# Kernel optimization log

Measured on AMD Instinct MI355X. Metric: run time of the kernel, lower is better.

Reference implementation:

```python
import jax, jax.numpy as jnp
import numpy as np

N_NODES = 100000


def _gcn_layer(x, W, b, src, dst, ew):
    # support = x @ W  (dense transform first, standard GCN)
    support = x @ W  # [N, out]
    # sparse propagate: out[i] = sum_{e: dst[e]=i} ew[e] * support[src[e]]
    msgs = support[src] * ew[:, None]  # [E, out]
    out = jax.ops.segment_sum(msgs, dst, num_segments=N_NODES)
    return out + b


def setup_inputs() -> dict:
    key = jax.random.key(0)
    ks = jax.random.split(key, 7)
    nfeat, nhid, nclass, E = 512, 256, 40, 3200000
    x = jax.random.normal(ks[0], (N_NODES, nfeat), dtype=jnp.float32)
    edge_index = jax.random.randint(ks[1], (2, E), 0, N_NODES, dtype=jnp.int32)
    edge_weight = jax.random.uniform(ks[2], (E,), dtype=jnp.float32)
    W1 = jax.random.normal(ks[3], (nfeat, nhid), dtype=jnp.float32) / np.sqrt(nfeat)
    b1 = jnp.zeros((nhid,), dtype=jnp.float32)
    W2 = jax.random.normal(ks[4], (nhid, nclass), dtype=jnp.float32) / np.sqrt(nhid)
    b2 = jnp.zeros((nclass,), dtype=jnp.float32)
    return {"x": x, "edge_index": edge_index, "edge_weight": edge_weight,
            "W1": W1, "b1": b1, "W2": W2, "b2": b2}


def reference(x, edge_index, edge_weight, W1, b1, W2, b2):
    src, dst = edge_index[0], edge_index[1]
    h = _gcn_layer(x, W1, b1, src, dst, edge_weight)
    h = jax.nn.relu(h)  # with_relu=True; dropout skipped (eval mode)
    h = _gcn_layer(h, W2, b2, src, dst, edge_weight)
    return jax.nn.log_softmax(h, axis=1)
```

## Files before the change

kernel.cpp:

```cpp
#include <hip/hip_runtime.h>
#include <math.h>

#define N_NODES 100000
#define M_PAD 100096
#define NFEAT 512
#define NHID 256
#define NCLASS 40
#define SUP2_LD 48

#define NBKT 250
#define NPB 400
#define BINA_CHUNK 3072
#define BCAP 14336

typedef __attribute__((ext_vector_type(8))) short bf16x8;
typedef __attribute__((ext_vector_type(4))) float f32x4;

__device__ __forceinline__ unsigned short f2bf(float f) {
    unsigned int u = __builtin_bit_cast(unsigned int, f);
    u += 0x7fffu + ((u >> 16) & 1u);
    return (unsigned short)(u >> 16);
}
__device__ __forceinline__ void bf2x2(unsigned int u, float& f0, float& f1) {
    f0 = __builtin_bit_cast(float, u << 16);
    f1 = __builtin_bit_cast(float, u & 0xffff0000u);
}
__device__ __forceinline__ void gload16(const void* g, void* l) {
    __builtin_amdgcn_global_load_lds(
        (const __attribute__((address_space(1))) unsigned int*)g,
        (__attribute__((address_space(3))) unsigned int*)l, 16, 0, 0);
}
template <int CODE>
__device__ __forceinline__ float swzx(float v) {
    return __builtin_bit_cast(float,
        __builtin_amdgcn_ds_swizzle(__builtin_bit_cast(int, v), CODE));
}

#define CVTW_BLOCKS 512

__global__ __launch_bounds__(256) void k_init(int* __restrict__ bcur,
                                              const float* __restrict__ W1,
                                              unsigned short* __restrict__ w1t,
                                              const float* __restrict__ W2,
                                              uint4* __restrict__ w2f) {
    int b = blockIdx.x;
    int t = threadIdx.x;
    if (b == 0) {
        if (t < NBKT) bcur[t] = t * BCAP;
    } else if (b <= CVTW_BLOCKS) {
        int idx = (b - 1) * 256 + t;
        int n = idx >> 9, k = idx & 511;
        w1t[idx] = f2bf(W1[(size_t)k * NHID + n]);
    } else {
        for (int idx = t; idx < 8 * 3 * 64; idx += 256) {
            int ks = idx / 192;
            int rem = idx - ks * 192;
            int n = rem >> 6;
            int l = rem & 63;
            int col = n * 16 + (l & 15);
            int kbase = ks * 32 + (l >> 4) * 8;
            unsigned short o[8];
#pragma unroll
            for (int j = 0; j < 8; ++j)
                o[j] = (col < NCLASS) ? f2bf(W2[(size_t)(kbase + j) * NCLASS + col]) : 0;
            w2f[idx] = *(const uint4*)o;
        }
    }
}

__device__ __forceinline__ void binA_body(char* smbase, int t, int cblk,
                                          const int* __restrict__ src,
                                          const int* __restrict__ dst,
                                          const float* __restrict__ ew,
                                          int* __restrict__ bcur,
                                          uint2* __restrict__ tmp, int E) {
    uint2* sorted = (uint2*)smbase;
    unsigned char* bkt8 = (unsigned char*)(smbase + 24576);
    int* cnt = (int*)(smbase + 27648);
    int* startv = cnt + 256;
    int* offv = startv + 256;
    int* gb = offv + 256;
    int c0 = cblk * BINA_CHUNK;
    int n = min(BINA_CHUNK, E - c0);
    cnt[t] = 0;
    __syncthreads();
    for (int j = t; j < n; j += 256) {
        atomicAdd(&cnt[(unsigned)dst[c0 + j] / NPB], 1);
    }
    __syncthreads();
    int v = cnt[t];
    startv[t] = v;
    __syncthreads();
    for (int o = 1; o < 256; o <<= 1) {
        int a = (t >= o) ? startv[t - o] : 0;
        __syncthreads();
        startv[t] += a;
        __syncthreads();
    }
    int ex = startv[t] - v;
    __syncthreads();
    startv[t] = ex;
    offv[t] = ex;
    if (t < NBKT) gb[t] = (v > 0) ? atomicAdd(&bcur[t], v) : 0;
    __syncthreads();
    for (int j = t; j < n; j += 256) {
        int d = dst[c0 + j];
        int b = (unsigned)d / NPB;
        int dl = d - b * NPB;
        int r = atomicAdd(&offv[b], 1);
        sorted[r] = make_uint2((unsigned)src[c0 + j] | ((unsigned)dl << 17),
                               __builtin_bit_cast(unsigned, ew[c0 + j]));
        bkt8[r] = (unsigned char)b;
    }
    __syncthreads();
    for (int j = t; j < n; j += 256) {
        int b = bkt8[j];
        tmp[gb[b] + (j - startv[b])] = sorted[j];
    }
}

__device__ __forceinline__ void gemm1_body(char* smem, int t, int mb,
                                           const float* __restrict__ x,
                                           const unsigned short* __restrict__ w1t,
                                           unsigned short* __restrict__ sup1) {
    const int w = t >> 6, lane = t & 63;
    const int m0 = mb * 128;
    const int wm = w >> 1, wn = w & 1;
    const int r15 = lane & 15, hi = lane >> 4;

    f32x4 acc[4][8];
#pragma unroll
    for (int i = 0; i < 4; ++i)
#pragma unroll
        for (int j = 0; j < 8; ++j) acc[i][j] = (f32x4){0.f, 0.f, 0.f, 0.f};

    const char* wsrc = (const char*)w1t;

#define STAGE1(kt, b)                                                                  \
    {                                                                                  \
        char* Ab = smem + (b) * 8192;                                                  \
        char* Bb = smem + 16384 + (b) * 16384;                                         \
        _Pragma("unroll") for (int i = 0; i < 2; ++i) {                                \
            int u = i * 256 + t;                                                       \
            int row = u >> 2, part = u & 3;                                            \
            int gr = m0 + row;                                                         \
            unsigned short ob[8];                                                      \
            if (gr < N_NODES) {                                                        \
                const float* sp = x + (size_t)gr * NFEAT + (kt) * 32 + part * 8;       \
                float4 v0 = *(const float4*)sp;                                        \
                float4 v1 = *(const float4*)(sp + 4);                                  \
                ob[0] = f2bf(v0.x); ob[1] = f2bf(v0.y);                                \
                ob[2] = f2bf(v0.z); ob[3] = f2bf(v0.w);                                \
                ob[4] = f2bf(v1.x); ob[5] = f2bf(v1.y);                                \
                ob[6] = f2bf(v1.z); ob[7] = f2bf(v1.w);                                \
            } else {                                                                   \
                _Pragma("unroll") for (int j = 0; j < 8; ++j) ob[j] = 0;               \
            }                                                                          \
            *(uint4*)(Ab + row * 64 + ((part ^ ((row >> 1) & 3)) << 4)) =              \
                *(const uint4*)ob;                                                     \
        }                                                                              \
        _Pragma("unroll") for (int i = 0; i < 4; ++i) {                                \
            int u = i * 256 + t;                                                       \
            int nrow = u >> 2, part = u & 3;                                           \
            int q = part ^ ((nrow >> 1) & 3);                                          \
            gload16(wsrc + (size_t)nrow * 1024 + (kt) * 64 + q * 16, Bb + u * 16);     \
        }                                                                              \
    }

    STAGE1(0, 0);
    for (int kt = 0; kt < 16; ++kt) {
        __syncthreads();
        if (kt < 15) STAGE1(kt + 1, (kt + 1) & 1);
        const char* Ab = smem + (kt & 1) * 8192;
        const char* Bb = smem + 16384 + (kt & 1) * 16384;
        bf16x8 a[4], bb[8];
#pragma unroll
        for (int i = 0; i < 4; ++i) {
            int r = wm * 64 + i * 16 + r15;
            a[i] = *(const bf16x8*)(Ab + r * 64 + ((hi ^ ((r >> 1) & 3)) << 4));
        }
#pragma unroll
        for (int j = 0; j < 8; ++j) {
            int n = wn * 128 + j * 16 + r15;
            bb[j] = *(const bf16x8*)(Bb + n * 64 + ((hi ^ ((n >> 1) & 3)) << 4));
        }
#pragma unroll
        for (int i = 0; i < 4; ++i)
#pragma unroll
            for (int j = 0; j < 8; ++j)
                acc[i][j] = __builtin_amdgcn_mfma_f32_16x16x32_bf16(a[i], bb[j], acc[i][j], 0, 0, 0);
    }
#undef STAGE1

#pragma unroll
    for (int i = 0; i < 4; ++i) {
        int rowb = m0 + wm * 64 + i * 16 + hi * 4;
#pragma unroll
        for (int j = 0; j < 8; ++j) {
            int col = wn * 128 + j * 16 + r15;
#pragma unroll
            for (int r = 0; r < 4; ++r)
                sup1[(size_t)(rowb + r) * NHID + col] = f2bf(acc[i][j][r]);
        }
    }
}

#define GEMM1_BLOCKS (M_PAD / 128)

__global__ __launch_bounds__(256) void k_fat(const float* __restrict__ x,
                                             const unsigned short* __restrict__ w1t,
                                             unsigned short* __restrict__ sup1,
                                             const int* __restrict__ src,
                                             const int* __restrict__ dst,
                                             const float* __restrict__ ew,
                                             int* __restrict__ bcur,
                                             uint2* __restrict__ tmp, int E) {
    __shared__ __align__(16) char smem[49152];
    int b = blockIdx.x;
    int t = threadIdx.x;
    if (b < GEMM1_BLOCKS) {
        gemm1_body(smem, t, b, x, w1t, sup1);
    } else {
        binA_body(smem, t, b - GEMM1_BLOCKS, src, dst, ew, bcur, tmp, E);
    }
}

__global__ __launch_bounds__(256) void k_binB(const uint2* __restrict__ tmp,
                                              const int* __restrict__ bcur,
                                              int* __restrict__ rowptr,
                                              uint2* __restrict__ cedge) {
    __shared__ int sc[256];
    __shared__ int nc[NPB];
    __shared__ int st[NPB];
    int b = blockIdx.x, t = threadIdx.x;
    int c = (t < NBKT) ? (bcur[t] - t * BCAP) : 0;
    sc[t] = c;
    __syncthreads();
    for (int o = 1; o < 256; o <<= 1) {
        int a = (t >= o) ? sc[t - o] : 0;
        __syncthreads();
        sc[t] += a;
        __syncthreads();
    }
    int base = (b == 0) ? 0 : sc[b - 1];
    int mycnt = sc[b] - base;
    int total = sc[NBKT - 1];
    __syncthreads();
    for (int i = t; i < NPB; i += 256) nc[i] = 0;
    __syncthreads();
    const uint2* srcp = tmp + (size_t)b * BCAP;
    for (int j = t; j < mycnt; j += 256) atomicAdd(&nc[srcp[j].x >> 17], 1);
    __syncthreads();
    int v0 = nc[t];
    sc[t] = v0;
    __syncthreads();
    for (int o = 1; o < 256; o <<= 1) {
        int a = (t >= o) ? sc[t - o] : 0;
        __syncthreads();
        sc[t] += a;
        __syncthreads();
    }
    int tot0 = sc[255];
    st[t] = sc[t] - v0;
    __syncthreads();
    int v1 = (t < NPB - 256) ? nc[256 + t] : 0;
    sc[t] = v1;
    __syncthreads();
    for (int o = 1; o < 256; o <<= 1) {
        int a = (t >= o) ? sc[t - o] : 0;
        __syncthreads();
        sc[t] += a;
        __syncthreads();
    }
    if (t < NPB - 256) st[256 + t] = tot0 + sc[t] - v1;
    __syncthreads();
    int n0 = b * NPB;
    for (int i = t; i < NPB; i += 256) {
        int s = base + st[i];
        rowptr[n0 + i] = s;
        st[i] = s;
    }
    if (b == NBKT - 1 && t == 0) rowptr[N_NODES] = total;
    __syncthreads();
    for (int j = t; j < mycnt; j += 256) {
        uint2 e = srcp[j];
        int dl = e.x >> 17;
        int addr = atomicAdd(&st[dl], 1);
        cedge[addr] = make_uint2(e.x & 0x1FFFFu, e.y);
    }
}

__global__ __launch_bounds__(256) void k_prop1(const unsigned short* __restrict__ sup1,
                                               const int* __restrict__ rowptr,
                                               const uint2* __restrict__ cedge,
                                               const float* __restrict__ b1,
                                               unsigned short* __restrict__ h1) {
    int gid = blockIdx.x * blockDim.x + threadIdx.x;
    int wid = gid >> 6;
    int lane = gid & 63;
    if (wid >= N_NODES) return;
    int beg = rowptr[wid], end = rowptr[wid + 1];
    float a0 = 0.f, a1 = 0.f, a2 = 0.f, a3 = 0.f;
    int e = beg;
    for (; e + 7 < end; e += 8) {
        uint2 ed[8];
#pragma unroll
        for (int q = 0; q < 8; ++q) ed[q] = cedge[e + q];
        uint2 r[8];
#pragma unroll
        for (int q = 0; q < 8; ++q)
            r[q] = *(const uint2*)(sup1 + (size_t)ed[q].x * NHID + lane * 4);
#pragma unroll
        for (int q = 0; q < 8; ++q) {
            float wq = __builtin_bit_cast(float, ed[q].y);
            float f0, f1, f2, f3;
            bf2x2(r[q].x, f0, f1);
            bf2x2(r[q].y, f2, f3);
            a0 += wq * f0; a1 += wq * f1; a2 += wq * f2; a3 += wq * f3;
        }
    }
    for (; e < end; ++e) {
        uint2 ed = cedge[e];
        float wq = __builtin_bit_cast(float, ed.y);
        uint2 rv = *(const uint2*)(sup1 + (size_t)ed.x * NHID + lane * 4);
        float f0, f1, f2, f3;
        bf2x2(rv.x, f0, f1);
        bf2x2(rv.y, f2, f3);
        a0 += wq * f0; a1 += wq * f1; a2 += wq * f2; a3 += wq * f3;
    }
    float4 bv = *(const float4*)(b1 + lane * 4);
    a0 = fmaxf(a0 + bv.x, 0.f);
    a1 = fmaxf(a1 + bv.y, 0.f);
    a2 = fmaxf(a2 + bv.z, 0.f);
    a3 = fmaxf(a3 + bv.w, 0.f);
    unsigned short o[4] = {f2bf(a0), f2bf(a1), f2bf(a2), f2bf(a3)};
    *(uint2*)(h1 + (size_t)wid * NHID + lane * 4) = *(const uint2*)o;
}

__global__ __launch_bounds__(256) void k_gemm2(const unsigned short* __restrict__ h1,
                                               const uint4* __restrict__ w2f,
                                               unsigned short* __restrict__ sup2) {
    int t = threadIdx.x;
    int w = t >> 6, lane = t & 63;
    int m0 = (blockIdx.x * 4 + w) * 16;
    int r15 = lane & 15, hi = lane >> 4;

    bf16x8 bfrag[8][3];
#pragma unroll
    for (int ks = 0; ks < 8; ++ks)
#pragma unroll
        for (int n = 0; n < 3; ++n)
            bfrag[ks][n] = __builtin_bit_cast(bf16x8, w2f[(ks * 3 + n) * 64 + lane]);

    f32x4 acc[3];
#pragma unroll
    for (int n = 0; n < 3; ++n) acc[n] = (f32x4){0.f, 0.f, 0.f, 0.f};

    const unsigned short* arow = h1 + (size_t)(m0 + r15) * NHID + hi * 8;
#pragma unroll
    for (int ks = 0; ks < 8; ++ks) {
        bf16x8 a = *(const bf16x8*)(arow + ks * 32);
#pragma unroll
        for (int n = 0; n < 3; ++n)
            acc[n] = __builtin_amdgcn_mfma_f32_16x16x32_bf16(a, bfrag[ks][n], acc[n], 0, 0, 0);
    }
#pragma unroll
    for (int n = 0; n < 3; ++n) {
        int col = n * 16 + r15;
#pragma unroll
        for (int r = 0; r < 4; ++r) {
            int row = m0 + hi * 4 + r;
            sup2[(size_t)row * SUP2_LD + col] = f2bf(acc[n][r]);
        }
    }
}

__global__ __launch_bounds__(256) void k_prop2(const unsigned short* __restrict__ sup2,
                                               const int* __restrict__ rowptr,
                                               const uint2* __restrict__ cedge,
                                               const float* __restrict__ b2,
                                               float* __restrict__ out) {
    int gid = blockIdx.x * blockDim.x + threadIdx.x;
    int wv = gid >> 6;
    int lane = gid & 63;
    int grp = lane >> 5;
    int l32 = lane & 31;
    int wid = wv * 2 + grp;
    if (wid >= N_NODES) return;
    int beg = rowptr[wid], end = rowptr[wid + 1];
    bool act = l32 < 20;
    int c2 = l32 * 2;
    float acc0 = 0.f, acc1 = 0.f;
    int e = beg;
    for (; e + 7 < end; e += 8) {
        uint2 ed[8];
#pragma unroll
        for (int q = 0; q < 8; ++q) ed[q] = cedge[e + q];
        unsigned u[8];
#pragma unroll
        for (int q = 0; q < 8; ++q)
            u[q] = act ? *(const unsigned*)(sup2 + (size_t)ed[q].x * SUP2_LD + c2) : 0u;
#pragma unroll
        for (int q = 0; q < 8; ++q) {
            float wq = __builtin_bit_cast(float, ed[q].y);
            float f0, f1;
            bf2x2(u[q], f0, f1);
            acc0 += wq * f0;
            acc1 += wq * f1;
        }
    }
    for (; e < end; ++e) {
        uint2 eq = cedge[e];
        unsigned u = act ? *(const unsigned*)(sup2 + (size_t)eq.x * SUP2_LD + c2) : 0u;
        float wq = __builtin_bit_cast(float, eq.y);
        float f0, f1;
        bf2x2(u, f0, f1);
        acc0 += wq * f0;
        acc1 += wq * f1;
    }
    float v0 = -INFINITY, v1 = -INFINITY;
    if (act) {
        float2 bb = *(const float2*)(b2 + c2);
        v0 = acc0 + bb.x;
        v1 = acc1 + bb.y;
    }
    float m = fmaxf(v0, v1);
    m = fmaxf(m, swzx<0x401F>(m));
    m = fmaxf(m, swzx<0x201F>(m));
    m = fmaxf(m, swzx<0x101F>(m));
    m = fmaxf(m, swzx<0x081F>(m));
    m = fmaxf(m, swzx<0x041F>(m));
    float s = act ? (expf(v0 - m) + expf(v1 - m)) : 0.f;
    s += swzx<0x401F>(s);
    s += swzx<0x201F>(s);
    s += swzx<0x101F>(s);
    s += swzx<0x081F>(s);
    s += swzx<0x041F>(s);
    if (act) {
        float ls = logf(s);
        float2 o = make_float2(v0 - m - ls, v1 - m - ls);
        *(float2*)(out + (size_t)wid * NCLASS + c2) = o;
    }
}


extern "C" void kernel_launch(void* const* d_in, const int* in_sizes, int n_in,
                              void* d_out, int out_size, void* d_ws, size_t ws_size,
                              hipStream_t stream) {
    const float* x = (const float*)d_in[0];
    const int* ei = (const int*)d_in[1];
    const float* ew = (const float*)d_in[2];
    const float* W1 = (const float*)d_in[3];
    const float* b1 = (const float*)d_in[4];
    const float* W2 = (const float*)d_in[5];
    const float* b2 = (const float*)d_in[6];
    float* out = (float*)d_out;

    int E = in_sizes[1] / 2;
    const int* src = ei;
    const int* dst = ei + E;

    char* w = (char*)d_ws;
    size_t off = 0;
    auto alloc = [&](size_t bytes) {
        void* p = w + off;
        off += (bytes + 255) & ~(size_t)255;
        return p;
    };
    unsigned short* w1t = (unsigned short*)alloc((size_t)NHID * NFEAT * 2);
    unsigned short* sup1 = (unsigned short*)alloc((size_t)M_PAD * NHID * 2);
    unsigned short* h1 = (unsigned short*)alloc((size_t)M_PAD * NHID * 2);
    uint2* cedge = (uint2*)alloc((size_t)E * 8);
    uint2* tmp = (uint2*)alloc((size_t)NBKT * BCAP * 8);
    unsigned short* sup2 = (unsigned short*)alloc((size_t)M_PAD * SUP2_LD * 2);
    int* rowptr = (int*)alloc((size_t)(N_NODES + 1) * 4);
    int* bcur = (int*)alloc((size_t)NBKT * 4);
    uint4* w2f = (uint4*)alloc((size_t)8 * 3 * 64 * 16);

    const int BINA_BLOCKS = (E + BINA_CHUNK - 1) / BINA_CHUNK;

    k_init<<<1 + CVTW_BLOCKS + 1, 256, 0, stream>>>(bcur, W1, w1t, W2, w2f);
    k_fat<<<GEMM1_BLOCKS + BINA_BLOCKS, 256, 0, stream>>>(x, w1t, sup1,
                                                          src, dst, ew, bcur, tmp, E);
    k_binB<<<NBKT, 256, 0, stream>>>(tmp, bcur, rowptr, cedge);
    k_prop1<<<(N_NODES + 3) / 4, 256, 0, stream>>>(sup1, rowptr, cedge, b1, h1);
    k_gemm2<<<M_PAD / 64, 256, 0, stream>>>(h1, w2f, sup2);
    k_prop2<<<(N_NODES / 2 + 3) / 4, 256, 0, stream>>>(sup2, rowptr, cedge, b2, out);
}
```

Baseline: 506.2 us.

## Give GEMM1 blocks two tiles each and pack four nodes per wave in prop2

```diff
diff --git a/kernel.cpp b/kernel.cpp
--- a/kernel.cpp
+++ b/kernel.cpp
@@ -12,6 +12,9 @@
 #define NPB 400
 #define BINA_CHUNK 3072
 #define BCAP 14336
+
+#define GEMM1_TILES 782
+#define GEMM1_BLOCKS 391
 
 typedef __attribute__((ext_vector_type(8))) short bf16x8;
 typedef __attribute__((ext_vector_type(4))) float f32x4;
@@ -205,8 +208,6 @@
     }
 }
 
-#define GEMM1_BLOCKS (M_PAD / 128)
-
 __global__ __launch_bounds__(256) void k_fat(const float* __restrict__ x,
                                              const unsigned short* __restrict__ w1t,
                                              unsigned short* __restrict__ sup1,
@@ -220,6 +221,8 @@
     int t = threadIdx.x;
     if (b < GEMM1_BLOCKS) {
         gemm1_body(smem, t, b, x, w1t, sup1);
+        __syncthreads();
+        gemm1_body(smem, t, b + GEMM1_BLOCKS, x, w1t, sup1);
     } else {
         binA_body(smem, t, b - GEMM1_BLOCKS, src, dst, ew, bcur, tmp, E);
     }
@@ -383,63 +386,65 @@
     int gid = blockIdx.x * blockDim.x + threadIdx.x;
     int wv = gid >> 6;
     int lane = gid & 63;
-    int grp = lane >> 5;
-    int l32 = lane & 31;
-    int wid = wv * 2 + grp;
+    int grp = lane >> 4;
+    int gl = lane & 15;
+    int wid = wv * 4 + grp;
     if (wid >= N_NODES) return;
     int beg = rowptr[wid], end = rowptr[wid + 1];
-    bool act = l32 < 20;
-    int c2 = l32 * 2;
-    float acc0 = 0.f, acc1 = 0.f;
+    bool act = gl < 10;
+    int c4 = gl * 4;
+    float acc0 = 0.f, acc1 = 0.f, acc2 = 0.f, acc3 = 0.f;
     int e = beg;
     for (; e + 7 < end; e += 8) {
         uint2 ed[8];
 #pragma unroll
         for (int q = 0; q < 8; ++q) ed[q] = cedge[e + q];
-        unsigned u[8];
+        uint2 u[8];
 #pragma unroll
         for (int q = 0; q < 8; ++q)
-            u[q] = act ? *(const unsigned*)(sup2 + (size_t)ed[q].x * SUP2_LD + c2) : 0u;
+            u[q] = act ? *(const uint2*)(sup2 + (size_t)ed[q].x * SUP2_LD + c4)
+                       : make_uint2(0u, 0u);
 #pragma unroll
         for (int q = 0; q < 8; ++q) {
             float wq = __builtin_bit_cast(float, ed[q].y);
-            float f0, f1;
-            bf2x2(u[q], f0, f1);
-            acc0 += wq * f0;
-            acc1 += wq * f1;
+            float f0, f1, f2, f3;
+            bf2x2(u[q].x, f0, f1);
+            bf2x2(u[q].y, f2, f3);
+            acc0 += wq * f0; acc1 += wq * f1; acc2 += wq * f2; acc3 += wq * f3;
         }
     }
     for (; e < end; ++e) {
         uint2 eq = cedge[e];
-        unsigned u = act ? *(const unsigned*)(sup2 + (size_t)eq.x * SUP2_LD + c2) : 0u;
+        uint2 u = act ? *(const uint2*)(sup2 + (size_t)eq.x * SUP2_LD + c4)
+                      : make_uint2(0u, 0u);
         float wq = __builtin_bit_cast(float, eq.y);
-        float f0, f1;
-        bf2x2(u, f0, f1);
-        acc0 += wq * f0;
-        acc1 += wq * f1;
-    }
-    float v0 = -INFINITY, v1 = -INFINITY;
+        float f0, f1, f2, f3;
+        bf2x2(u.x, f0, f1);
+        bf2x2(u.y, f2, f3);
+        acc0 += wq * f0; acc1 += wq * f1; acc2 += wq * f2; acc3 += wq * f3;
+    }
+    float v0 = -INFINITY, v1 = -INFINITY, v2 = -INFINITY, v3 = -INFINITY;
     if (act) {
-        float2 bb = *(const float2*)(b2 + c2);
+        float4 bb = *(const float4*)(b2 + c4);
         v0 = acc0 + bb.x;
         v1 = acc1 + bb.y;
-    }
-    float m = fmaxf(v0, v1);
-    m = fmaxf(m, swzx<0x401F>(m));
+        v2 = acc2 + bb.z;
+        v3 = acc3 + bb.w;
+    }
+    float m = fmaxf(fmaxf(v0, v1), fmaxf(v2, v3));
     m = fmaxf(m, swzx<0x201F>(m));
     m = fmaxf(m, swzx<0x101F>(m));
     m = fmaxf(m, swzx<0x081F>(m));
     m = fmaxf(m, swzx<0x041F>(m));
-    float s = act ? (expf(v0 - m) + expf(v1 - m)) : 0.f;
-    s += swzx<0x401F>(s);
+    float s = act ? (expf(v0 - m) + expf(v1 - m) + expf(v2 - m) + expf(v3 - m)) : 0.f;
     s += swzx<0x201F>(s);
     s += swzx<0x101F>(s);
     s += swzx<0x081F>(s);
     s += swzx<0x041F>(s);
     if (act) {
         float ls = logf(s);
-        float2 o = make_float2(v0 - m - ls, v1 - m - ls);
-        *(float2*)(out + (size_t)wid * NCLASS + c2) = o;
+        float4 o = make_float4(v0 - m - ls, v1 - m - ls, v2 - m - ls, v3 - m - ls);
+        *(float4*)(out + (size_t)wid * NCLASS + c4) = o;
     }
 }
 
@@ -485,5 +490,5 @@
     k_binB<<<NBKT, 256, 0, stream>>>(tmp, bcur, rowptr, cedge);
     k_prop1<<<(N_NODES + 3) / 4, 256, 0, stream>>>(sup1, rowptr, cedge, b1, h1);
     k_gemm2<<<M_PAD / 64, 256, 0, stream>>>(h1, w2f, sup2);
-    k_prop2<<<(N_NODES / 2 + 3) / 4, 256, 0, stream>>>(sup2, rowptr, cedge, b2, out);
-}
+    k_prop2<<<(N_NODES / 4 + 3) / 4, 256, 0, stream>>>(sup2, rowptr, cedge, b2, out);
+}
```

Result: slower. 544.2 us (+7.5%).
